# Kernel optimization log

Hardware: AMD Instinct MI355X
Metric: run time of the kernel (lower is better)

Reference implementation:

```python
import jax, jax.numpy as jnp
import numpy as np

D_MODEL = 1024
NUM_HEADS = 16
D_HEAD = D_MODEL // NUM_HEADS
MAX_DISTANCE = 128
SEQ_LEN = 2048


def setup_inputs() -> dict:
    key = jax.random.key(0)
    k_x, k_qkv, k_out, k_bias = jax.random.split(key, 4)
    scale = 1.0 / np.sqrt(D_MODEL)
    return {
        "x": jax.random.normal(k_x, (SEQ_LEN, D_MODEL), dtype=jnp.float32),
        "w_qkv": jax.random.normal(k_qkv, (D_MODEL, 3 * D_MODEL), dtype=jnp.float32) * scale,
        "w_out": jax.random.normal(k_out, (D_MODEL, D_MODEL), dtype=jnp.float32) * scale,
        "rel_bias": jax.random.normal(k_bias, (MAX_DISTANCE, NUM_HEADS), dtype=jnp.float32) * 0.02,
    }


def _position_bias(rel_bias, seq_len):
    # relative_position[q, k] = k - q; bucket = clip(|rel|, 0, max_distance-1)
    ctx = jnp.arange(seq_len)[:, None]
    mem = jnp.arange(seq_len)[None, :]
    bucket = jnp.clip(jnp.abs(mem - ctx), 0, MAX_DISTANCE - 1)  # [q, k]
    return rel_bias[bucket]  # [q, k, h]


def reference(x, w_qkv, w_out, rel_bias):
    seq_len = x.shape[0]
    qkv = x @ w_qkv  # [s, 3*d_model]
    q, k, v = jnp.split(qkv, 3, axis=-1)
    q = q.reshape(seq_len, NUM_HEADS, D_HEAD)
    k = k.reshape(seq_len, NUM_HEADS, D_HEAD)
    v = v.reshape(seq_len, NUM_HEADS, D_HEAD)
    bias = _position_bias(rel_bias, seq_len)  # [q, k, h]
    # flax dot_product_attention semantics: scale q by 1/sqrt(d_head), add bias, softmax over kv
    scores = jnp.einsum("qhd,khd->hqk", q, k) / jnp.sqrt(jnp.asarray(D_HEAD, q.dtype))
    scores = scores + jnp.transpose(bias, (2, 0, 1))  # [h, q, k]
    weights = jax.nn.softmax(scores, axis=-1)
    attn = jnp.einsum("hqk,khd->qhd", weights, v)  # [s, h, d_head]
    attn = attn.reshape(1, seq_len, D_MODEL)
    return attn @ w_out  # [1, s, d_model]
```

## Files before the change

kernel.cpp:

```cpp
#include <hip/hip_runtime.h>
#include <hip/hip_bf16.h>

#define SEQ   2048
#define DM    1024
#define NH    16
#define DH    64
#define MAXD  128

typedef __attribute__((ext_vector_type(8))) short  short8;
typedef __attribute__((ext_vector_type(4))) float  float4v;

__device__ __forceinline__ short8 ld8(const void* p) {
    short8 v; __builtin_memcpy(&v, p, 16); return v;
}
__device__ __forceinline__ void st8(void* p, short8 v) {
    __builtin_memcpy(p, &v, 16);
}
__device__ __forceinline__ short bf16bits(float f) {
    __hip_bfloat16 b = __float2bfloat16(f);
    short s; __builtin_memcpy(&s, &b, 2); return s;
}
__device__ __forceinline__ float bits2f(short s) {
    unsigned u = (unsigned)(unsigned short)s << 16;
    return __builtin_bit_cast(float, u);
}

__device__ __forceinline__ void async16(void* lds, const void* g) {
    __builtin_amdgcn_global_load_lds(
        (const __attribute__((address_space(1))) unsigned int*)g,
        (__attribute__((address_space(3))) unsigned int*)lds, 16, 0, 0);
}

template <int CTRL>
__device__ __forceinline__ float dppmov(float x) {
    return __builtin_bit_cast(float,
        __builtin_amdgcn_update_dpp(0, __builtin_bit_cast(int, x), CTRL, 0xf, 0xf, true));
}
__device__ __forceinline__ float red16max(float x) {
    x = fmaxf(x, dppmov<0xB1>(x));
    x = fmaxf(x, dppmov<0x4E>(x));
    x = fmaxf(x, dppmov<0x141>(x));
    x = fmaxf(x, dppmov<0x140>(x));
    return x;
}
__device__ __forceinline__ float red16sum(float x) {
    x += dppmov<0xB1>(x);
    x += dppmov<0x4E>(x);
    x += dppmov<0x141>(x);
    x += dppmov<0x140>(x);
    return x;
}

__global__ __launch_bounds__(256) void prep_kernel(
    const float* __restrict__ wq, const float* __restrict__ wo,
    const float* __restrict__ x,
    __hip_bfloat16* __restrict__ wqT, __hip_bfloat16* __restrict__ woT,
    __hip_bfloat16* __restrict__ xb) {
    const int t = threadIdx.x;
    const int bx = blockIdx.x;
    if (bx >= 128) {
        const size_t id = (size_t)(bx - 128) * 32 + blockIdx.y;
        const size_t i  = id * 2048 + t * 8;
        float f[8]; __builtin_memcpy(f, x + i, 32);
        short8 v;
#pragma unroll
        for (int j = 0; j < 8; ++j) v[j] = bf16bits(f[j]);
        st8(xb + i, v);
        return;
    }
    __shared__ __hip_bfloat16 tile[32][33];
    const int tx = t % 32, ty = t / 32;
    const int r0 = blockIdx.y * 32;
    const float* src; __hip_bfloat16* dst; int ss, ds, c0;
    if (bx < 96) { src = wq; dst = wqT; ss = 3 * DM; ds = DM; c0 = bx * 32; }
    else         { src = wo; dst = woT; ss = DM;     ds = DM; c0 = (bx - 96) * 32; }
#pragma unroll
    for (int i = 0; i < 4; ++i)
        tile[ty + i * 8][tx] = __float2bfloat16(src[(size_t)(r0 + ty + i * 8) * ss + c0 + tx]);
    __syncthreads();
#pragma unroll
    for (int i = 0; i < 4; ++i)
        dst[(size_t)(c0 + ty + i * 8) * ds + r0 + tx] = tile[tx][ty + i * 8];
}

__global__ __launch_bounds__(256) void transpose_v(
    const __hip_bfloat16* __restrict__ src, __hip_bfloat16* __restrict__ dst,
    int s_stride, int d_stride) {
    __shared__ __hip_bfloat16 tile[32][33];
    const int t = threadIdx.x;
    const int tx = t % 32, ty = t / 32;
    const int c0 = blockIdx.x * 32, r0 = blockIdx.y * 32;
#pragma unroll
    for (int i = 0; i < 4; ++i)
        tile[ty + i * 8][tx] = src[(size_t)(r0 + ty + i * 8) * s_stride + c0 + tx];
    __syncthreads();
#pragma unroll
    for (int i = 0; i < 4; ++i)
        dst[(size_t)(c0 + ty + i * 8) * d_stride + r0 + tx] = tile[tx][ty + i * 8];
}

template <int NT, typename TC>
__global__ __launch_bounds__(256) void gemm_mfma(
    const __hip_bfloat16* __restrict__ A,
    const __hip_bfloat16* __restrict__ BT,
    TC* __restrict__ C,
    int M, int N, int K) {
    __shared__ short As[128 * 32];
    __shared__ short Bs[32 * NT * 32];

    const int t = threadIdx.x;
    const int w = t >> 6, lane = t & 63;
    const int l15 = lane & 15, quad = lane >> 4;
    const int row0 = blockIdx.y * 128;
    const int col0 = blockIdx.x * (32 * NT);
    const int wm = w >> 1, wn = w & 1;

    float4v acc[4][NT];
#pragma unroll
    for (int i = 0; i < 4; ++i)
#pragma unroll
        for (int j = 0; j < NT; ++j) acc[i][j] = (float4v){0.f, 0.f, 0.f, 0.f};

    const int mloc0 = lane >> 2;
    const int u     = lane & 3;

    for (int k0 = 0; k0 < K; k0 += 32) {
#pragma unroll
        for (int i = 0; i < 2; ++i) {
            const int c = 2 * w + i;
            async16(&As[c * 512], A + (size_t)(row0 + c * 16 + mloc0) * K + k0 + u * 8);
        }
#pragma unroll
        for (int i = 0; i < NT / 2; ++i) {
            const int c = (NT / 2) * w + i;
            async16(&Bs[c * 512], BT + (size_t)(col0 + c * 16 + mloc0) * K + k0 + u * 8);
        }
        __syncthreads();

        short8 af[4], bf[NT];
#pragma unroll
        for (int mt = 0; mt < 4; ++mt)
            af[mt] = ld8(&As[(wm * 64 + mt * 16 + l15) * 32 + quad * 8]);
#pragma unroll
        for (int nt = 0; nt < NT; ++nt)
            bf[nt] = ld8(&Bs[(wn * 16 * NT + nt * 16 + l15) * 32 + quad * 8]);
#pragma unroll
        for (int mt = 0; mt < 4; ++mt)
#pragma unroll
            for (int nt = 0; nt < NT; ++nt)
                acc[mt][nt] = __builtin_amdgcn_mfma_f32_16x16x32_bf16(
                    af[mt], bf[nt], acc[mt][nt], 0, 0, 0);
        __syncthreads();
    }

#pragma unroll
    for (int mt = 0; mt < 4; ++mt)
#pragma unroll
        for (int nt = 0; nt < NT; ++nt)
#pragma unroll
            for (int r = 0; r < 4; ++r) {
                const int row = row0 + wm * 64 + mt * 16 + quad * 4 + r;
                const int col = col0 + wn * 16 * NT + nt * 16 + l15;
                float v = acc[mt][nt][r];
                if constexpr (__is_same(TC, float)) C[(size_t)row * N + col] = v;
                else C[(size_t)row * N + col] = __float2bfloat16(v);
            }
}

__global__ __launch_bounds__(256) void gemm64(
    const __hip_bfloat16* __restrict__ A,
    const __hip_bfloat16* __restrict__ BT,
    float* __restrict__ C,
    int M, int N, int K) {
    __shared__ short As[64 * 32];
    __shared__ short Bs[64 * 32];

    const int t = threadIdx.x;
    const int w = t >> 6, lane = t & 63;
    const int l15 = lane & 15, quad = lane >> 4;
    const int row0 = blockIdx.y * 64;
    const int col0 = blockIdx.x * 64;
    const int wm = w >> 1, wn = w & 1;

    float4v acc[2][2];
#pragma unroll
    for (int i = 0; i < 2; ++i)
#pragma unroll
        for (int j = 0; j < 2; ++j) acc[i][j] = (float4v){0.f, 0.f, 0.f, 0.f};

    const int mloc0 = lane >> 2;
    const int u     = lane & 3;

    for (int k0 = 0; k0 < K; k0 += 32) {
        async16(&As[w * 512], A  + (size_t)(row0 + w * 16 + mloc0) * K + k0 + u * 8);
        async16(&Bs[w * 512], BT + (size_t)(col0 + w * 16 + mloc0) * K + k0 + u * 8);
        __syncthreads();

        short8 af[2], bf[2];
#pragma unroll
        for (int mt = 0; mt < 2; ++mt)
            af[mt] = ld8(&As[(wm * 32 + mt * 16 + l15) * 32 + quad * 8]);
#pragma unroll
        for (int nt = 0; nt < 2; ++nt)
            bf[nt] = ld8(&Bs[(wn * 32 + nt * 16 + l15) * 32 + quad * 8]);
#pragma unroll
        for (int mt = 0; mt < 2; ++mt)
#pragma unroll
            for (int nt = 0; nt < 2; ++nt)
                acc[mt][nt] = __builtin_amdgcn_mfma_f32_16x16x32_bf16(
                    af[mt], bf[nt], acc[mt][nt], 0, 0, 0);
        __syncthreads();
    }

#pragma unroll
    for (int mt = 0; mt < 2; ++mt)
#pragma unroll
        for (int nt = 0; nt < 2; ++nt)
#pragma unroll
            for (int r = 0; r < 4; ++r) {
                const int row = row0 + wm * 32 + mt * 16 + quad * 4 + r;
                const int col = col0 + wn * 32 + nt * 16 + l15;
                C[(size_t)row * N + col] = acc[mt][nt][r];
            }
}

#define TK  128
#define KS  68
#define VS  132

__global__ __launch_bounds__(256) void attn_mfma(
    const __hip_bfloat16* __restrict__ qkv,
    const __hip_bfloat16* __restrict__ vT,
    const float* __restrict__ rel_bias,
    __hip_bfloat16* __restrict__ attnb) {
    __shared__ short Kt[TK * KS];
    __shared__ short Vt[DH * VS];
    __shared__ short Pl[4 * 16 * VS];
    __shared__ float biasL[MAXD];

    const int t = threadIdx.x;
    const int w = t >> 6, lane = t & 63;
    const int l15 = lane & 15, quad = lane >> 4;
    const int h  = blockIdx.y;
    const int q0 = blockIdx.x * 64;
    const int qw = q0 + w * 16;

    if (t < MAXD) biasL[t] = rel_bias[t * NH + h];

    short8 qf[2];
#pragma unroll
    for (int c = 0; c < 2; ++c) {
        short8 raw = ld8(qkv + (size_t)(qw + l15) * (3 * DM) + h * DH + c * 32 + quad * 8);
#pragma unroll
        for (int j = 0; j < 8; ++j) qf[c][j] = bf16bits(bits2f(raw[j]) * 0.125f);
    }

    float4v o_acc[4];
#pragma unroll
    for (int nt = 0; nt < 4; ++nt) o_acc[nt] = (float4v){0.f, 0.f, 0.f, 0.f};
    float m_i[4], l_i[4];
#pragma unroll
    for (int r = 0; r < 4; ++r) { m_i[r] = -1e30f; l_i[r] = 0.f; }

    for (int kb = 0; kb < SEQ / TK; ++kb) {
        const int k0 = kb * TK;
#pragma unroll
        for (int p = 0; p < 4; ++p) {
            const int idx = p * 256 + t;
            const int row = idx >> 3, u = idx & 7;
            st8(&Kt[row * KS + u * 8],
                ld8(qkv + (size_t)(k0 + row) * (3 * DM) + DM + h * DH + u * 8));
        }
#pragma unroll
        for (int p = 0; p < 4; ++p) {
            const int idx = p * 256 + t;
            const int row = idx >> 4, u = idx & 15;
            st8(&Vt[row * VS + u * 8],
                ld8(vT + (size_t)(h * DH + row) * SEQ + k0 + u * 8));
        }
        __syncthreads();

        float4v s_acc[8];
#pragma unroll
        for (int kt = 0; kt < 8; ++kt) s_acc[kt] = (float4v){0.f, 0.f, 0.f, 0.f};
#pragma unroll
        for (int c = 0; c < 2; ++c)
#pragma unroll
            for (int kt = 0; kt < 8; ++kt) {
                short8 kf = ld8(&Kt[(kt * 16 + l15) * KS + (c * 4 + quad) * 8]);
                s_acc[kt] = __builtin_amdgcn_mfma_f32_16x16x32_bf16(qf[c], kf, s_acc[kt], 0, 0, 0);
            }

        float sv[8][4];
        const int dlo = k0 - (qw + 15);
        const int dhi = qw - (k0 + TK - 1);
        if (dlo >= MAXD - 1 || dhi >= MAXD - 1) {
            const float bu = biasL[MAXD - 1];
#pragma unroll
            for (int kt = 0; kt < 8; ++kt)
#pragma unroll
                for (int r = 0; r < 4; ++r) sv[kt][r] = s_acc[kt][r] + bu;
        } else {
#pragma unroll
            for (int kt = 0; kt < 8; ++kt)
#pragma unroll
                for (int r = 0; r < 4; ++r) {
                    const int kg = k0 + kt * 16 + l15;
                    const int qg = qw + quad * 4 + r;
                    int rel = kg - qg; if (rel < 0) rel = -rel;
                    if (rel > MAXD - 1) rel = MAXD - 1;
                    sv[kt][r] = s_acc[kt][r] + biasL[rel];
                }
        }

        float rowm[4];
#pragma unroll
        for (int r = 0; r < 4; ++r) {
            float m = sv[0][r];
#pragma unroll
            for (int kt = 1; kt < 8; ++kt) m = fmaxf(m, sv[kt][r]);
            rowm[r] = red16max(m);
        }

        float al[4], rs[4];
#pragma unroll
        for (int r = 0; r < 4; ++r) {
            const float mn = fmaxf(m_i[r], rowm[r]);
            al[r] = __expf(m_i[r] - mn);
            m_i[r] = mn;
            rs[r] = 0.f;
        }
#pragma unroll
        for (int kt = 0; kt < 8; ++kt)
#pragma unroll
            for (int r = 0; r < 4; ++r) {
                const float p = __expf(sv[kt][r] - m_i[r]);
                sv[kt][r] = p;
                rs[r] += p;
            }
#pragma unroll
        for (int r = 0; r < 4; ++r) {
            rs[r] = red16sum(rs[r]);
            l_i[r] = l_i[r] * al[r] + rs[r];
        }
#pragma unroll
        for (int nt = 0; nt < 4; ++nt)
#pragma unroll
            for (int r = 0; r < 4; ++r) o_acc[nt][r] *= al[r];

#pragma unroll
        for (int kt = 0; kt < 8; ++kt)
#pragma unroll
            for (int r = 0; r < 4; ++r)
                Pl[w * 16 * VS + (quad * 4 + r) * VS + kt * 16 + l15] = bf16bits(sv[kt][r]);

#pragma unroll
        for (int kc = 0; kc < 4; ++kc) {
            short8 pf = ld8(&Pl[w * 16 * VS + l15 * VS + kc * 32 + quad * 8]);
#pragma unroll
            for (int nt = 0; nt < 4; ++nt) {
                short8 vf = ld8(&Vt[(nt * 16 + l15) * VS + kc * 32 + quad * 8]);
                o_acc[nt] = __builtin_amdgcn_mfma_f32_16x16x32_bf16(pf, vf, o_acc[nt], 0, 0, 0);
            }
        }
        __syncthreads();
    }

#pragma unroll
    for (int nt = 0; nt < 4; ++nt)
#pragma unroll
        for (int r = 0; r < 4; ++r) {
            const int row = qw + quad * 4 + r;
            const int col = h * DH + nt * 16 + l15;
            attnb[(size_t)row * DM + col] = __float2bfloat16(o_acc[nt][r] / l_i[r]);
        }
}

extern "C" void kernel_launch(void* const* d_in, const int* in_sizes, int n_in,
                              void* d_out, int out_size, void* d_ws, size_t ws_size,
                              hipStream_t stream) {
    const float* x        = (const float*)d_in[0];
    const float* w_qkv    = (const float*)d_in[1];
    const float* w_out    = (const float*)d_in[2];
    const float* rel_bias = (const float*)d_in[3];
    float* out = (float*)d_out;

    char* p = (char*)d_ws;
    __hip_bfloat16* xb    = (__hip_bfloat16*)p;  p += (size_t)SEQ * DM * 2;
    __hip_bfloat16* wqT   = (__hip_bfloat16*)p;  p += (size_t)3 * DM * DM * 2;
    __hip_bfloat16* woT   = (__hip_bfloat16*)p;  p += (size_t)DM * DM * 2;
    __hip_bfloat16* qkvb  = (__hip_bfloat16*)p;  p += (size_t)SEQ * 3 * DM * 2;
    __hip_bfloat16* vT    = (__hip_bfloat16*)p;  p += (size_t)DM * SEQ * 2;
    __hip_bfloat16* attnb = (__hip_bfloat16*)p;

    prep_kernel<<<dim3(160, 32), 256, 0, stream>>>(w_qkv, w_out, x, wqT, woT, xb);

    gemm_mfma<2, __hip_bfloat16><<<dim3(3 * DM / 64, SEQ / 128), 256, 0, stream>>>(
        xb, wqT, qkvb, SEQ, 3 * DM, DM);

    transpose_v<<<dim3(DM / 32, SEQ / 32), 256, 0, stream>>>(
        qkvb + 2 * DM, vT, 3 * DM, SEQ);

    attn_mfma<<<dim3(SEQ / 64, NH), 256, 0, stream>>>(qkvb, vT, rel_bias, attnb);

    gemm64<<<dim3(DM / 64, SEQ / 64), 256, 0, stream>>>(
        attnb, woT, out, SEQ, DM, DM);
}
```

Measured before the change: 169.7 us.

## Fuse V transpose into attention load, deepen GEMM K-step, use fast bf16 rounding

Removes the separate transpose_v kernel and its vT buffer. The attention kernel now reads V straight from the qkv buffer and scatters it transposed into LDS. Both GEMMs load two 32-wide K chunks per barrier pair, halving the synchronisation count per K. P is converted to bf16 with a cheap add-and-shift instead of the library conversion. Costs: the scattered LDS stores for V may cause bank conflicts, and the fast rounding does not handle NaN or exact round-to-nearest-even ties.

```diff
diff --git a/kernel.cpp b/kernel.cpp
--- a/kernel.cpp
+++ b/kernel.cpp
@@ -19,6 +19,10 @@
 __device__ __forceinline__ short bf16bits(float f) {
     __hip_bfloat16 b = __float2bfloat16(f);
     short s; __builtin_memcpy(&s, &b, 2); return s;
+}
+__device__ __forceinline__ short bf16fast(float f) {
+    unsigned u = __builtin_bit_cast(unsigned, f);
+    return (short)((u + 0x8000u) >> 16);
 }
 __device__ __forceinline__ float bits2f(short s) {
     unsigned u = (unsigned)(unsigned short)s << 16;
@@ -83,97 +87,82 @@
         dst[(size_t)(c0 + ty + i * 8) * ds + r0 + tx] = tile[tx][ty + i * 8];
 }
 
-__global__ __launch_bounds__(256) void transpose_v(
-    const __hip_bfloat16* __restrict__ src, __hip_bfloat16* __restrict__ dst,
-    int s_stride, int d_stride) {
-    __shared__ __hip_bfloat16 tile[32][33];
-    const int t = threadIdx.x;
-    const int tx = t % 32, ty = t / 32;
-    const int c0 = blockIdx.x * 32, r0 = blockIdx.y * 32;
-#pragma unroll
-    for (int i = 0; i < 4; ++i)
-        tile[ty + i * 8][tx] = src[(size_t)(r0 + ty + i * 8) * s_stride + c0 + tx];
-    __syncthreads();
-#pragma unroll
-    for (int i = 0; i < 4; ++i)
-        dst[(size_t)(c0 + ty + i * 8) * d_stride + r0 + tx] = tile[tx][ty + i * 8];
-}
-
-template <int NT, typename TC>
-__global__ __launch_bounds__(256) void gemm_mfma(
+__global__ __launch_bounds__(256) void gemm_qkv(
     const __hip_bfloat16* __restrict__ A,
     const __hip_bfloat16* __restrict__ BT,
-    TC* __restrict__ C,
+    __hip_bfloat16* __restrict__ C,
     int M, int N, int K) {
-    __shared__ short As[128 * 32];
-    __shared__ short Bs[32 * NT * 32];
+    __shared__ short As[2 * 128 * 32];
+    __shared__ short Bs[2 * 64 * 32];
 
     const int t = threadIdx.x;
     const int w = t >> 6, lane = t & 63;
     const int l15 = lane & 15, quad = lane >> 4;
     const int row0 = blockIdx.y * 128;
-    const int col0 = blockIdx.x * (32 * NT);
+    const int col0 = blockIdx.x * 64;
     const int wm = w >> 1, wn = w & 1;
 
-    float4v acc[4][NT];
+    float4v acc[4][2];
 #pragma unroll
     for (int i = 0; i < 4; ++i)
 #pragma unroll
-        for (int j = 0; j < NT; ++j) acc[i][j] = (float4v){0.f, 0.f, 0.f, 0.f};
+        for (int j = 0; j < 2; ++j) acc[i][j] = (float4v){0.f, 0.f, 0.f, 0.f};
 
     const int mloc0 = lane >> 2;
     const int u     = lane & 3;
 
-    for (int k0 = 0; k0 < K; k0 += 32) {
-#pragma unroll
-        for (int i = 0; i < 2; ++i) {
-            const int c = 2 * w + i;
-            async16(&As[c * 512], A + (size_t)(row0 + c * 16 + mloc0) * K + k0 + u * 8);
-        }
-#pragma unroll
-        for (int i = 0; i < NT / 2; ++i) {
-            const int c = (NT / 2) * w + i;
-            async16(&Bs[c * 512], BT + (size_t)(col0 + c * 16 + mloc0) * K + k0 + u * 8);
-        }
-        __syncthreads();
-
-        short8 af[4], bf[NT];
-#pragma unroll
-        for (int mt = 0; mt < 4; ++mt)
-            af[mt] = ld8(&As[(wm * 64 + mt * 16 + l15) * 32 + quad * 8]);
-#pragma unroll
-        for (int nt = 0; nt < NT; ++nt)
-            bf[nt] = ld8(&Bs[(wn * 16 * NT + nt * 16 + l15) * 32 + quad * 8]);
-#pragma unroll
-        for (int mt = 0; mt < 4; ++mt)
-#pragma unroll
-            for (int nt = 0; nt < NT; ++nt)
-                acc[mt][nt] = __builtin_amdgcn_mfma_f32_16x16x32_bf16(
-                    af[mt], bf[nt], acc[mt][nt], 0, 0, 0);
+    for (int k0 = 0; k0 < K; k0 += 64) {
+#pragma unroll
+        for (int kc = 0; kc < 2; ++kc) {
+#pragma unroll
+            for (int i = 0; i < 2; ++i) {
+                const int c = 2 * w + i;
+                async16(&As[kc * 4096 + c * 512],
+                        A + (size_t)(row0 + c * 16 + mloc0) * K + k0 + kc * 32 + u * 8);
+            }
+            async16(&Bs[kc * 2048 + w * 512],
+                    BT + (size_t)(col0 + w * 16 + mloc0) * K + k0 + kc * 32 + u * 8);
+        }
+        __syncthreads();
+
+#pragma unroll
+        for (int kc = 0; kc < 2; ++kc) {
+            short8 af[4], bf[2];
+#pragma unroll
+            for (int mt = 0; mt < 4; ++mt)
+                af[mt] = ld8(&As[kc * 4096 + (wm * 64 + mt * 16 + l15) * 32 + quad * 8]);
+#pragma unroll
+            for (int nt = 0; nt < 2; ++nt)
+                bf[nt] = ld8(&Bs[kc * 2048 + (wn * 32 + nt * 16 + l15) * 32 + quad * 8]);
+#pragma unroll
+            for (int mt = 0; mt < 4; ++mt)
+#pragma unroll
+                for (int nt = 0; nt < 2; ++nt)
+                    acc[mt][nt] = __builtin_amdgcn_mfma_f32_16x16x32_bf16(
+                        af[mt], bf[nt], acc[mt][nt], 0, 0, 0);
+        }
         __syncthreads();
     }
 
 #pragma unroll
     for (int mt = 0; mt < 4; ++mt)
 #pragma unroll
-        for (int nt = 0; nt < NT; ++nt)
+        for (int nt = 0; nt < 2; ++nt)
 #pragma unroll
             for (int r = 0; r < 4; ++r) {
                 const int row = row0 + wm * 64 + mt * 16 + quad * 4 + r;
-                const int col = col0 + wn * 16 * NT + nt * 16 + l15;
-                float v = acc[mt][nt][r];
-                if constexpr (__is_same(TC, float)) C[(size_t)row * N + col] = v;
-                else C[(size_t)row * N + col] = __float2bfloat16(v);
-            }
-}
-
-__global__ __launch_bounds__(256) void gemm64(
+                const int col = col0 + wn * 32 + nt * 16 + l15;
+                C[(size_t)row * N + col] = __float2bfloat16(acc[mt][nt][r]);
+            }
+}
+
+__global__ __launch_bounds__(256) void gemm_out(
     const __hip_bfloat16* __restrict__ A,
     const __hip_bfloat16* __restrict__ BT,
     float* __restrict__ C,
     int M, int N, int K) {
-    __shared__ short As[64 * 32];
-    __shared__ short Bs[64 * 32];
+    __shared__ short As[2 * 64 * 32];
+    __shared__ short Bs[2 * 64 * 32];
 
     const int t = threadIdx.x;
     const int w = t >> 6, lane = t & 63;
@@ -191,24 +180,32 @@
     const int mloc0 = lane >> 2;
     const int u     = lane & 3;
 
-    for (int k0 = 0; k0 < K; k0 += 32) {
-        async16(&As[w * 512], A  + (size_t)(row0 + w * 16 + mloc0) * K + k0 + u * 8);
-        async16(&Bs[w * 512], BT + (size_t)(col0 + w * 16 + mloc0) * K + k0 + u * 8);
-        __syncthreads();
-
-        short8 af[2], bf[2];
-#pragma unroll
-        for (int mt = 0; mt < 2; ++mt)
-            af[mt] = ld8(&As[(wm * 32 + mt * 16 + l15) * 32 + quad * 8]);
-#pragma unroll
-        for (int nt = 0; nt < 2; ++nt)
-            bf[nt] = ld8(&Bs[(wn * 32 + nt * 16 + l15) * 32 + quad * 8]);
-#pragma unroll
-        for (int mt = 0; mt < 2; ++mt)
+    for (int k0 = 0; k0 < K; k0 += 64) {
+#pragma unroll
+        for (int kc = 0; kc < 2; ++kc) {
+            async16(&As[kc * 2048 + w * 512],
+                    A + (size_t)(row0 + w * 16 + mloc0) * K + k0 + kc * 32 + u * 8);
+            async16(&Bs[kc * 2048 + w * 512],
+                    BT + (size_t)(col0 + w * 16 + mloc0) * K + k0 + kc * 32 + u * 8);
+        }
+        __syncthreads();
+
+#pragma unroll
+        for (int kc = 0; kc < 2; ++kc) {
+            short8 af[2], bf[2];
+#pragma unroll
+            for (int mt = 0; mt < 2; ++mt)
+                af[mt] = ld8(&As[kc * 2048 + (wm * 32 + mt * 16 + l15) * 32 + quad * 8]);
 #pragma unroll
             for (int nt = 0; nt < 2; ++nt)
-                acc[mt][nt] = __builtin_amdgcn_mfma_f32_16x16x32_bf16(
-                    af[mt], bf[nt], acc[mt][nt], 0, 0, 0);
+                bf[nt] = ld8(&Bs[kc * 2048 + (wn * 32 + nt * 16 + l15) * 32 + quad * 8]);
+#pragma unroll
+            for (int mt = 0; mt < 2; ++mt)
+#pragma unroll
+                for (int nt = 0; nt < 2; ++nt)
+                    acc[mt][nt] = __builtin_amdgcn_mfma_f32_16x16x32_bf16(
+                        af[mt], bf[nt], acc[mt][nt], 0, 0, 0);
+        }
         __syncthreads();
     }
 
@@ -230,7 +227,6 @@
 
 __global__ __launch_bounds__(256) void attn_mfma(
     const __hip_bfloat16* __restrict__ qkv,
-    const __hip_bfloat16* __restrict__ vT,
     const float* __restrict__ rel_bias,
     __hip_bfloat16* __restrict__ attnb) {
     __shared__ short Kt[TK * KS];
@@ -270,13 +266,10 @@
             const int row = idx >> 3, u = idx & 7;
             st8(&Kt[row * KS + u * 8],
                 ld8(qkv + (size_t)(k0 + row) * (3 * DM) + DM + h * DH + u * 8));
-        }
-#pragma unroll
-        for (int p = 0; p < 4; ++p) {
-            const int idx = p * 256 + t;
-            const int row = idx >> 4, u = idx & 15;
-            st8(&Vt[row * VS + u * 8],
-                ld8(vT + (size_t)(h * DH + row) * SEQ + k0 + u * 8));
+            short8 vv = ld8(qkv + (size_t)(k0 + row) * (3 * DM) + 2 * DM + h * DH + u * 8);
+#pragma unroll
+            for (int j = 0; j < 8; ++j)
+                Vt[(u * 8 + j) * VS + row] = vv[j];
         }
         __syncthreads();
 
@@ -352,7 +345,7 @@
         for (int kt = 0; kt < 8; ++kt)
 #pragma unroll
             for (int r = 0; r < 4; ++r)
-                Pl[w * 16 * VS + (quad * 4 + r) * VS + kt * 16 + l15] = bf16bits(sv[kt][r]);
+                Pl[w * 16 * VS + (quad * 4 + r) * VS + kt * 16 + l15] = bf16fast(sv[kt][r]);
 
 #pragma unroll
         for (int kc = 0; kc < 4; ++kc) {
@@ -390,19 +383,15 @@
     __hip_bfloat16* wqT   = (__hip_bfloat16*)p;  p += (size_t)3 * DM * DM * 2;
     __hip_bfloat16* woT   = (__hip_bfloat16*)p;  p += (size_t)DM * DM * 2;
     __hip_bfloat16* qkvb  = (__hip_bfloat16*)p;  p += (size_t)SEQ * 3 * DM * 2;
-    __hip_bfloat16* vT    = (__hip_bfloat16*)p;  p += (size_t)DM * SEQ * 2;
     __hip_bfloat16* attnb = (__hip_bfloat16*)p;
 
     prep_kernel<<<dim3(160, 32), 256, 0, stream>>>(w_qkv, w_out, x, wqT, woT, xb);
 
-    gemm_mfma<2, __hip_bfloat16><<<dim3(3 * DM / 64, SEQ / 128), 256, 0, stream>>>(
+    gemm_qkv<<<dim3(3 * DM / 64, SEQ / 128), 256, 0, stream>>>(
         xb, wqT, qkvb, SEQ, 3 * DM, DM);
 
-    transpose_v<<<dim3(DM / 32, SEQ / 32), 256, 0, stream>>>(
-        qkvb + 2 * DM, vT, 3 * DM, SEQ);
-
-    attn_mfma<<<dim3(SEQ / 64, NH), 256, 0, stream>>>(qkvb, vT, rel_bias, attnb);
-
-    gemm64<<<dim3(DM / 64, SEQ / 64), 256, 0, stream>>>(
+    attn_mfma<<<dim3(SEQ / 64, NH), 256, 0, stream>>>(qkvb, rel_bias, attnb);
+
+    gemm_out<<<dim3(DM / 64, SEQ / 64), 256, 0, stream>>>(
         attnb, woT, out, SEQ, DM, DM);
 }
```

New measurement: 171.2 us. Within noise of the previous version (+0.9%).
